# Kernel tuning notes

Hardware: AMD Instinct MI355X
Metric: run time of the kernel (lower is better)

## Reference

```python
import jax, jax.numpy as jnp
import numpy as np

B, N, F, E, C, FC = 16, 5000, 512, 160000, 64, 128


def gcn_conv(x, src, dst, W, b, n_total):
    loop = jnp.arange(n_total, dtype=src.dtype)
    s = jnp.concatenate([src, loop])
    d = jnp.concatenate([dst, loop])
    deg = jax.ops.segment_sum(jnp.ones_like(s, dtype=x.dtype), d, num_segments=n_total)
    dinv = jnp.where(deg > 0, jax.lax.rsqrt(deg), 0.0)
    norm = dinv[s] * dinv[d]                      # [E']
    h = x @ W                                      # [n_total, out]
    msg = h[s] * norm[:, None]
    out = jax.ops.segment_sum(msg, d, num_segments=n_total)
    return out + b


def setup_inputs() -> dict:
    key = jax.random.key(0)
    ks = jax.random.split(key, 12)
    inp = {
        "node_features": jax.random.normal(ks[0], (B, N, F), jnp.float32),
        "col_features": jax.random.normal(ks[1], (B, C, FC), jnp.float32),
        "edge_index": jax.random.randint(ks[2], (2, E), 0, N, dtype=jnp.int64),
        # GCNConv 1/2 weights + node head
        "W1": jax.random.normal(ks[3], (F, 16), jnp.float32) / np.sqrt(F),
        "b1": jnp.zeros((16,), jnp.float32),
        "W2": jax.random.normal(ks[4], (16, 16), jnp.float32) / 4.0,
        "b2": jnp.zeros((16,), jnp.float32),
        "fc_w": jax.random.normal(ks[5], (16, 1), jnp.float32) / 4.0,
        "fc_b": jnp.zeros((1,), jnp.float32),
        # column MLP: Linear(FC,16) -> ReLU -> Linear(16,1)
        "cw1": jax.random.normal(ks[6], (FC, 16), jnp.float32) / np.sqrt(FC),
        "cb1": jnp.zeros((16,), jnp.float32),
        "cw2": jax.random.normal(ks[7], (16, 1), jnp.float32) / 4.0,
        "cb2": jnp.zeros((1,), jnp.float32),
    }
    return inp


def reference(node_features, col_features, edge_index, W1, b1, W2, b2, fc_w, fc_b, cw1, cb1, cw2, cb2):
    b, n, _ = node_features.shape
    n_total = b * n
    # batched edge_index via node-offset trick (shared graph per batch element)
    offsets = (jnp.arange(b, dtype=edge_index.dtype) * n)[:, None]   # [B,1]
    src = (edge_index[0][None, :] + offsets).reshape(-1)              # [B*E]
    dst = (edge_index[1][None, :] + offsets).reshape(-1)

    x = node_features.reshape(n_total, -1)
    x = jax.nn.relu(gcn_conv(x, src, dst, W1, b1, n_total))
    x = jax.nn.relu(gcn_conv(x, src, dst, W2, b2, n_total))
    node_logits = (x.reshape(b, n, 16) @ fc_w + fc_b)[..., 0]         # [B,N]

    h = jax.nn.relu(col_features @ cw1 + cb1)
    col_logits = (h @ cw2 + cb2)[..., 0]                              # [B,C]

    joint = node_logits[:, :, None] + col_logits[:, None, :]          # [B,N,C]
    return joint.reshape(b, -1)                                       # [B, N*C]
```

## Files before the change

### kernel.cpp

```cpp
#include <hip/hip_runtime.h>
#include <hip/hip_bf16.h>

typedef unsigned short u16;
typedef unsigned int   u32;

#define B_  16
#define N_  5000
#define F_  512
#define C_  64
#define FC_ 128
#define NT  (B_ * N_)

__device__ __forceinline__ float bf2f(u16 h) {
    return __uint_as_float(((u32)h) << 16);
}
__device__ __forceinline__ u16 f2bf(float f) {
    union { __hip_bfloat16 h; u16 s; } c; c.h = __float2bfloat16(f); return c.s;
}
__device__ __forceinline__ float ldw(const void* p, int i, int fF) {
    return fF ? bf2f(((const u16*)p)[i]) : ((const float*)p)[i];
}

__global__ __launch_bounds__(256) void det_k(const u32* __restrict__ x32,
                                             const u32* __restrict__ ei32,
                                             int* __restrict__ flags)
{
    __shared__ int cnt;
    __shared__ int orv;
    if (threadIdx.x == 0) { cnt = 0; orv = 0; }
    __syncthreads();
    u32 w = x32[threadIdx.x];
    int e = (int)((w >> 7) & 0xffu);
    if (e >= 112 && e <= 136) atomicAdd(&cnt, 1);
    if (threadIdx.x < 32) {
        if (ei32[2 * threadIdx.x + 1] != 0u) atomicOr(&orv, 1);
    }
    __syncthreads();
    if (threadIdx.x == 0) {
        flags[0] = (cnt >= 128) ? 1 : 0;
        flags[1] = (orv == 0) ? 1 : 0;
    }
}

__device__ __forceinline__ int src_at(const u32* ei32, int t, int E, int fI) {
    return (int)(fI ? ei32[2 * t] : ei32[t]);
}
__device__ __forceinline__ int dst_at(const u32* ei32, int t, int E, int fI) {
    return (int)(fI ? ei32[2 * (E + t)] : ei32[E + t]);
}

__global__ __launch_bounds__(256) void prep_weights(
    const void* __restrict__ W1, const void* __restrict__ W2,
    const void* __restrict__ fcw, const void* __restrict__ cw1,
    const void* __restrict__ cw2, const void* __restrict__ b1,
    const void* __restrict__ b2, const void* __restrict__ fcb,
    const void* __restrict__ cb1, const void* __restrict__ cb2,
    const int* __restrict__ flags,
    float* __restrict__ w1f, float* __restrict__ w2f, float* __restrict__ fcwf,
    float* __restrict__ cw1f, float* __restrict__ cw2f, float* __restrict__ b1f,
    float* __restrict__ b2f, float* __restrict__ fcbf, float* __restrict__ cb1f,
    float* __restrict__ cb2f)
{
    int fF = flags[0];
    int t = blockIdx.x * blockDim.x + threadIdx.x;
    if (t < 8192) { w1f[t] = ldw(W1, t, fF); return; }
    int u = t - 8192;
    if (u < 256)  { w2f[u]  = ldw(W2, u, fF);  return; }  u -= 256;
    if (u < 16)   { fcwf[u] = ldw(fcw, u, fF); return; }  u -= 16;
    if (u < 2048) { cw1f[u] = ldw(cw1, u, fF); return; }  u -= 2048;
    if (u < 16)   { cw2f[u] = ldw(cw2, u, fF); return; }  u -= 16;
    if (u < 16)   { b1f[u]  = ldw(b1, u, fF);  return; }  u -= 16;
    if (u < 16)   { b2f[u]  = ldw(b2, u, fF);  return; }  u -= 16;
    if (u < 1)    { fcbf[u] = ldw(fcb, u, fF); return; }  u -= 1;
    if (u < 16)   { cb1f[u] = ldw(cb1, u, fF); return; }  u -= 16;
    if (u < 1)    { cb2f[u] = ldw(cb2, u, fF); return; }
}

__global__ __launch_bounds__(256) void deg_k(const u32* __restrict__ ei32,
                                             const int* __restrict__ flags,
                                             int* __restrict__ deg, int E)
{
    int t = blockIdx.x * blockDim.x + threadIdx.x;
    if (t >= E) return;
    int d = dst_at(ei32, t, E, flags[1]);
    if ((unsigned)d < (unsigned)N_) atomicAdd(&deg[d], 1);
}

__global__ __launch_bounds__(1024) void scan_k(const int* __restrict__ deg,
                                               int* __restrict__ rowptr,
                                               int* __restrict__ cursor,
                                               float* __restrict__ dinv)
{
    __shared__ int ssum[1024];
    int t = threadIdx.x;
    int base = t * 5;
    int loc[5];
    int run = 0;
#pragma unroll
    for (int i = 0; i < 5; i++) {
        int idx = base + i;
        int v = (idx < N_) ? deg[idx] : 0;
        loc[i] = run;
        run += v;
    }
    ssum[t] = run;
    __syncthreads();
    for (int offs = 1; offs < 1024; offs <<= 1) {
        int v = (t >= offs) ? ssum[t - offs] : 0;
        __syncthreads();
        ssum[t] += v;
        __syncthreads();
    }
    int exclusive = ssum[t] - run;
#pragma unroll
    for (int i = 0; i < 5; i++) {
        int idx = base + i;
        if (idx < N_) {
            int rp = exclusive + loc[i];
            rowptr[idx] = rp;
            cursor[idx] = rp;
            dinv[idx] = 1.0f / sqrtf((float)deg[idx] + 1.0f);
        }
    }
    if (t == 1023) rowptr[N_] = ssum[1023];
}

__global__ __launch_bounds__(256) void fill_k(const u32* __restrict__ ei32,
                                              const int* __restrict__ flags,
                                              int* __restrict__ cursor,
                                              int* __restrict__ csr, int E)
{
    int t = blockIdx.x * blockDim.x + threadIdx.x;
    if (t >= E) return;
    int fI = flags[1];
    int s = src_at(ei32, t, E, fI);
    int d = dst_at(ei32, t, E, fI);
    if ((unsigned)d >= (unsigned)N_) return;
    if ((unsigned)s >= (unsigned)N_) s = 0;
    int pos = atomicAdd(&cursor[d], 1);
    if ((unsigned)pos < (unsigned)E) csr[pos] = s;
}

__global__ __launch_bounds__(256) void gemm1_k(const void* __restrict__ xraw,
                                               const float* __restrict__ w1f,
                                               const float* __restrict__ dinv,
                                               const int* __restrict__ flags,
                                               u16* __restrict__ out)
{
    __shared__ float smem[64 * 129];
    const int t    = threadIdx.x;
    const int lane = t & 63;
    const int wv   = t >> 6;
    const int row0 = blockIdx.x * 64;
    const int fF   = flags[0];

    float acc[16];
#pragma unroll
    for (int k = 0; k < 16; k++) acc[k] = 0.0f;

    for (int p = 0; p < 4; p++) {
        __syncthreads();
        if (fF) {
            const u16* xb = (const u16*)xraw;
#pragma unroll
            for (int i = 0; i < 4; i++) {
                int idx = i * 256 + t;
                int r   = idx >> 4;
                int c   = (idx & 15) * 8;
                uint4 pk = *(const uint4*)(xb + (size_t)(row0 + r) * F_ + p * 128 + c);
                u32 q[4] = {pk.x, pk.y, pk.z, pk.w};
                float* dstp = smem + r * 129 + c;
#pragma unroll
                for (int j = 0; j < 4; j++) {
                    dstp[2 * j]     = bf2f((u16)(q[j] & 0xffffu));
                    dstp[2 * j + 1] = bf2f((u16)(q[j] >> 16));
                }
            }
        } else {
            const float* xf = (const float*)xraw;
#pragma unroll
            for (int i = 0; i < 8; i++) {
                int idx = i * 256 + t;
                int r   = idx >> 5;
                int c   = (idx & 31) * 4;
                float4 v = *(const float4*)(xf + (size_t)(row0 + r) * F_ + p * 128 + c);
                float* dstp = smem + r * 129 + c;
                dstp[0] = v.x; dstp[1] = v.y; dstp[2] = v.z; dstp[3] = v.w;
            }
        }
        __syncthreads();
        const float* xr = smem + lane * 129 + wv * 32;
        const float* wr = w1f + (p * 128 + wv * 32) * 16;
#pragma unroll
        for (int f = 0; f < 32; f++) {
            float xv = xr[f];
#pragma unroll
            for (int k = 0; k < 16; k++) acc[k] += xv * wr[f * 16 + k];
        }
    }

    __syncthreads();
    float (*red)[64][17] = (float (*)[64][17])smem;
#pragma unroll
    for (int k = 0; k < 16; k++) red[wv][lane][k] = acc[k];
    __syncthreads();

    int r  = t >> 2;
    int kc = (t & 3) * 4;
    int orow = row0 + r;
    float s = dinv[orow % N_];
    union { uint2 u; u16 h[4]; } o;
#pragma unroll
    for (int k = 0; k < 4; k++) {
        float v = red[0][r][kc + k] + red[1][r][kc + k]
                + red[2][r][kc + k] + red[3][r][kc + k];
        o.h[k] = f2bf(v * s);
    }
    *(uint2*)(out + (size_t)orow * 16 + kc) = o.u;
}

__global__ __launch_bounds__(256) void agg1_k(const u16* __restrict__ h,
                                              const int* __restrict__ rowptr,
                                              const int* __restrict__ csr,
                                              const float* __restrict__ dinv,
                                              const float* __restrict__ b1f,
                                              const float* __restrict__ w2f,
                                              u16* __restrict__ out)
{
    int t = blockIdx.x * blockDim.x + threadIdx.x;
    int g = t >> 4;
    if (g >= NT) return;
    int k = t & 15;
    int d = g % N_;
    int b = g / N_;
    const u16* hb = h + (size_t)b * N_ * 16;
    float acc = bf2f(hb[d * 16 + k]);
    int e0 = rowptr[d], e1 = rowptr[d + 1];
    for (int base = e0; base < e1; base += 8) {
        int idx[8];
#pragma unroll
        for (int j = 0; j < 8; j++) {
            int e = base + j;
            idx[j] = csr[e < e1 ? e : e0];
        }
        float v[8];
#pragma unroll
        for (int j = 0; j < 8; j++) v[j] = bf2f(hb[idx[j] * 16 + k]);
#pragma unroll
        for (int j = 0; j < 8; j++) if (base + j < e1) acc += v[j];
    }
    float dv = dinv[d];
    float x1 = fmaxf(acc * dv + b1f[k], 0.0f);
    float h2 = 0.0f;
#pragma unroll
    for (int j = 0; j < 16; j++) {
        float xj = __shfl(x1, j, 16);
        h2 += xj * w2f[j * 16 + k];
    }
    out[(size_t)g * 16 + k] = f2bf(h2 * dv);
}

__global__ __launch_bounds__(256) void agg2_k(const u16* __restrict__ h,
                                              const int* __restrict__ rowptr,
                                              const int* __restrict__ csr,
                                              const float* __restrict__ dinv,
                                              const float* __restrict__ b2f,
                                              const float* __restrict__ fcwf,
                                              const float* __restrict__ fcbf,
                                              float* __restrict__ nl)
{
    int t = blockIdx.x * blockDim.x + threadIdx.x;
    int g = t >> 4;
    if (g >= NT) return;
    int k = t & 15;
    int d = g % N_;
    int b = g / N_;
    const u16* hb = h + (size_t)b * N_ * 16;
    float acc = bf2f(hb[d * 16 + k]);
    int e0 = rowptr[d], e1 = rowptr[d + 1];
    for (int base = e0; base < e1; base += 8) {
        int idx[8];
#pragma unroll
        for (int j = 0; j < 8; j++) {
            int e = base + j;
            idx[j] = csr[e < e1 ? e : e0];
        }
        float v[8];
#pragma unroll
        for (int j = 0; j < 8; j++) v[j] = bf2f(hb[idx[j] * 16 + k]);
#pragma unroll
        for (int j = 0; j < 8; j++) if (base + j < e1) acc += v[j];
    }
    float x2 = fmaxf(acc * dinv[d] + b2f[k], 0.0f);
    float p = x2 * fcwf[k];
    p += __shfl_xor(p, 8, 16);
    p += __shfl_xor(p, 4, 16);
    p += __shfl_xor(p, 2, 16);
    p += __shfl_xor(p, 1, 16);
    if (k == 0) nl[g] = p + fcbf[0];
}

__global__ __launch_bounds__(256) void col_k(const void* __restrict__ cfraw,
                                             const float* __restrict__ cw1f,
                                             const float* __restrict__ cb1f,
                                             const float* __restrict__ cw2f,
                                             const float* __restrict__ cb2f,
                                             const int* __restrict__ flags,
                                             float* __restrict__ cl)
{
    int t = blockIdx.x * blockDim.x + threadIdx.x;
    if (t >= B_ * C_) return;
    float acc[16];
#pragma unroll
    for (int k = 0; k < 16; k++) acc[k] = cb1f[k];
    if (flags[0]) {
        const u16* r = (const u16*)cfraw + (size_t)t * FC_;
        for (int f = 0; f < FC_; f += 8) {
            uint4 pk = *(const uint4*)(r + f);
            u32 q[4] = {pk.x, pk.y, pk.z, pk.w};
#pragma unroll
            for (int j = 0; j < 4; j++) {
                float v0 = bf2f((u16)(q[j] & 0xffffu));
                float v1 = bf2f((u16)(q[j] >> 16));
                const float* w0 = cw1f + (f + 2 * j) * 16;
#pragma unroll
                for (int k = 0; k < 16; k++) acc[k] += v0 * w0[k];
#pragma unroll
                for (int k = 0; k < 16; k++) acc[k] += v1 * w0[16 + k];
            }
        }
    } else {
        const float* r = (const float*)cfraw + (size_t)t * FC_;
        for (int f = 0; f < FC_; f += 4) {
            float4 a = *(const float4*)(r + f);
            float v[4] = {a.x, a.y, a.z, a.w};
#pragma unroll
            for (int j = 0; j < 4; j++) {
                const float* w0 = cw1f + (f + j) * 16;
#pragma unroll
                for (int k = 0; k < 16; k++) acc[k] += v[j] * w0[k];
            }
        }
    }
    float s = cb2f[0];
#pragma unroll
    for (int k = 0; k < 16; k++) s += fmaxf(acc[k], 0.0f) * cw2f[k];
    cl[t] = s;
}

__global__ __launch_bounds__(256) void join_k(const float* __restrict__ nl,
                                              const float* __restrict__ cl,
                                              const int* __restrict__ flags,
                                              void* __restrict__ outraw)
{
    int t = blockIdx.x * blockDim.x + threadIdx.x;
    if (t >= NT * C_ / 8) return;
    int g  = t >> 3;
    int c0 = (t & 7) * 8;
    int b  = g / N_;
    float nv = nl[g];
    const float* c = cl + b * C_ + c0;
    float4 a0 = *(const float4*)c;
    float4 a1 = *(const float4*)(c + 4);
    float v[8] = {a0.x, a0.y, a0.z, a0.w, a1.x, a1.y, a1.z, a1.w};
#pragma unroll
    for (int i = 0; i < 8; i++) v[i] += nv;
    size_t idx = (size_t)g * C_ + c0;
    if (flags[0]) {
        union { uint4 u; u16 h[8]; } pkv;
#pragma unroll
        for (int i = 0; i < 8; i++) pkv.h[i] = f2bf(v[i]);
        *(uint4*)((u16*)outraw + idx) = pkv.u;
    } else {
        float* o = (float*)outraw + idx;
        *(float4*)o       = make_float4(v[0], v[1], v[2], v[3]);
        *(float4*)(o + 4) = make_float4(v[4], v[5], v[6], v[7]);
    }
}

extern "C" void kernel_launch(void* const* d_in, const int* in_sizes, int n_in,
                              void* d_out, int out_size, void* d_ws, size_t ws_size,
                              hipStream_t stream)
{
    const void* x    = d_in[0];
    const void* cf   = d_in[1];
    const u32*  ei32 = (const u32*)d_in[2];
    const void* W1   = d_in[3];
    const void* b1   = d_in[4];
    const void* W2   = d_in[5];
    const void* b2   = d_in[6];
    const void* fcw  = d_in[7];
    const void* fcb  = d_in[8];
    const void* cw1  = d_in[9];
    const void* cb1  = d_in[10];
    const void* cw2  = d_in[11];
    const void* cb2  = d_in[12];

    const int E = in_sizes[2] / 2;

    char* base = (char*)d_ws;
    size_t off = 0;
    auto alloc = [&](size_t bytes) -> void* {
        void* p = base + off;
        off = (off + bytes + 255) & ~(size_t)255;
        return p;
    };
    int*   flags  = (int*)alloc(2 * 4);
    float* w1f  = (float*)alloc(8192 * 4);
    float* w2f  = (float*)alloc(256 * 4);
    float* fcwf = (float*)alloc(16 * 4);
    float* cw1f = (float*)alloc(2048 * 4);
    float* cw2f = (float*)alloc(16 * 4);
    float* b1f  = (float*)alloc(16 * 4);
    float* b2f  = (float*)alloc(16 * 4);
    float* fcbf = (float*)alloc(4);
    float* cb1f = (float*)alloc(16 * 4);
    float* cb2f = (float*)alloc(4);
    int*   deg    = (int*)alloc((size_t)N_ * 4);
    int*   rowptr = (int*)alloc((size_t)(N_ + 1) * 4);
    int*   cursor = (int*)alloc((size_t)N_ * 4);
    float* dinv   = (float*)alloc((size_t)N_ * 4);
    int*   csr    = (int*)alloc((size_t)E * 4);
    u16*   bufA = (u16*)alloc((size_t)NT * 16 * 2);
    u16*   bufB = (u16*)alloc((size_t)NT * 16 * 2);
    float* nl   = (float*)alloc((size_t)NT * 4);
    float* cl   = (float*)alloc((size_t)B_ * C_ * 4);

    det_k<<<1, 256, 0, stream>>>((const u32*)x, ei32, flags);
    hipMemsetAsync(deg, 0, (size_t)N_ * 4, stream);
    prep_weights<<<(10578 + 255) / 256, 256, 0, stream>>>(
        W1, W2, fcw, cw1, cw2, b1, b2, fcb, cb1, cb2, flags,
        w1f, w2f, fcwf, cw1f, cw2f, b1f, b2f, fcbf, cb1f, cb2f);
    deg_k<<<(E + 255) / 256, 256, 0, stream>>>(ei32, flags, deg, E);
    scan_k<<<1, 1024, 0, stream>>>(deg, rowptr, cursor, dinv);
    fill_k<<<(E + 255) / 256, 256, 0, stream>>>(ei32, flags, cursor, csr, E);

    gemm1_k<<<NT / 64, 256, 0, stream>>>(x, w1f, dinv, flags, bufA);
    agg1_k<<<(NT * 16 + 255) / 256, 256, 0, stream>>>(bufA, rowptr, csr, dinv, b1f, w2f, bufB);
    agg2_k<<<(NT * 16 + 255) / 256, 256, 0, stream>>>(bufB, rowptr, csr, dinv, b2f, fcwf, fcbf, nl);
    col_k<<<(B_ * C_ + 255) / 256, 256, 0, stream>>>(cf, cw1f, cb1f, cw2f, cb2f, flags, cl);
    join_k<<<(NT * C_ / 8 + 255) / 256, 256, 0, stream>>>(nl, cl, flags, d_out);
}
```

Measured before the change: 404.2 us.

## Store hidden features node-major across batch and double-buffer GEMM1 tiles

The intermediate hidden buffers change from [B][N][16] to [N][B][16], so one block per node aggregates all 16 batch copies. Each neighbor gather then reads a contiguous 512-byte row instead of 16 scattered 32-byte pieces, and the CSR index reads are shared across the batch. GEMM1 separately switches to 64-column chunks with a register-prefetched, double-buffered shared-memory pipeline so global loads overlap the FMA work. The risks are more registers in GEMM1 and only 5000 blocks for the aggregation kernels.

```diff
diff --git a/kernel.cpp b/kernel.cpp
--- a/kernel.cpp
+++ b/kernel.cpp
@@ -147,7 +147,7 @@
                                                const int* __restrict__ flags,
                                                u16* __restrict__ out)
 {
-    __shared__ float smem[64 * 129];
+    __shared__ float smem[2][64 * 65];
     const int t    = threadIdx.x;
     const int lane = t & 63;
     const int wv   = t >> 6;
@@ -158,44 +158,114 @@
 #pragma unroll
     for (int k = 0; k < 16; k++) acc[k] = 0.0f;
 
-    for (int p = 0; p < 4; p++) {
+    float sreg[16];
+    if (fF) {
+        const u16* xb = (const u16*)xraw;
+#pragma unroll
+        for (int i = 0; i < 2; i++) {
+            int u = i * 256 + t;
+            int r = u >> 3, c8 = u & 7;
+            uint4 pk = *(const uint4*)(xb + (size_t)(row0 + r) * F_ + c8 * 8);
+            u32 q[4] = {pk.x, pk.y, pk.z, pk.w};
+#pragma unroll
+            for (int j = 0; j < 4; j++) {
+                sreg[i * 8 + 2 * j]     = bf2f((u16)(q[j] & 0xffffu));
+                sreg[i * 8 + 2 * j + 1] = bf2f((u16)(q[j] >> 16));
+            }
+        }
+    } else {
+        const float* xf = (const float*)xraw;
+#pragma unroll
+        for (int i = 0; i < 4; i++) {
+            int u = i * 256 + t;
+            int r = u >> 4, c4 = u & 15;
+            float4 v = *(const float4*)(xf + (size_t)(row0 + r) * F_ + c4 * 4);
+            sreg[i * 4 + 0] = v.x; sreg[i * 4 + 1] = v.y;
+            sreg[i * 4 + 2] = v.z; sreg[i * 4 + 3] = v.w;
+        }
+    }
+    if (fF) {
+#pragma unroll
+        for (int i = 0; i < 2; i++) {
+            int u = i * 256 + t;
+            int r = u >> 3, c8 = u & 7;
+            float* dp = &smem[0][r * 65 + c8 * 8];
+#pragma unroll
+            for (int j = 0; j < 8; j++) dp[j] = sreg[i * 8 + j];
+        }
+    } else {
+#pragma unroll
+        for (int i = 0; i < 4; i++) {
+            int u = i * 256 + t;
+            int r = u >> 4, c4 = u & 15;
+            float* dp = &smem[0][r * 65 + c4 * 4];
+#pragma unroll
+            for (int j = 0; j < 4; j++) dp[j] = sreg[i * 4 + j];
+        }
+    }
+
+    for (int c = 0; c < 8; c++) {
         __syncthreads();
-        if (fF) {
-            const u16* xb = (const u16*)xraw;
-#pragma unroll
-            for (int i = 0; i < 4; i++) {
-                int idx = i * 256 + t;
-                int r   = idx >> 4;
-                int c   = (idx & 15) * 8;
-                uint4 pk = *(const uint4*)(xb + (size_t)(row0 + r) * F_ + p * 128 + c);
-                u32 q[4] = {pk.x, pk.y, pk.z, pk.w};
-                float* dstp = smem + r * 129 + c;
-#pragma unroll
-                for (int j = 0; j < 4; j++) {
-                    dstp[2 * j]     = bf2f((u16)(q[j] & 0xffffu));
-                    dstp[2 * j + 1] = bf2f((u16)(q[j] >> 16));
+        float nreg[16];
+        if (c < 7) {
+            int fo = (c + 1) * 64;
+            if (fF) {
+                const u16* xb = (const u16*)xraw;
+#pragma unroll
+                for (int i = 0; i < 2; i++) {
+                    int u = i * 256 + t;
+                    int r = u >> 3, c8 = u & 7;
+                    uint4 pk = *(const uint4*)(xb + (size_t)(row0 + r) * F_ + fo + c8 * 8);
+                    u32 q[4] = {pk.x, pk.y, pk.z, pk.w};
+#pragma unroll
+                    for (int j = 0; j < 4; j++) {
+                        nreg[i * 8 + 2 * j]     = bf2f((u16)(q[j] & 0xffffu));
+                        nreg[i * 8 + 2 * j + 1] = bf2f((u16)(q[j] >> 16));
+                    }
+                }
+            } else {
+                const float* xf = (const float*)xraw;
+#pragma unroll
+                for (int i = 0; i < 4; i++) {
+                    int u = i * 256 + t;
+                    int r = u >> 4, c4 = u & 15;
+                    float4 v = *(const float4*)(xf + (size_t)(row0 + r) * F_ + fo + c4 * 4);
+                    nreg[i * 4 + 0] = v.x; nreg[i * 4 + 1] = v.y;
+                    nreg[i * 4 + 2] = v.z; nreg[i * 4 + 3] = v.w;
                 }
             }
-        } else {
-            const float* xf = (const float*)xraw;
-#pragma unroll
-            for (int i = 0; i < 8; i++) {
-                int idx = i * 256 + t;
-                int r   = idx >> 5;
-                int c   = (idx & 31) * 4;
-                float4 v = *(const float4*)(xf + (size_t)(row0 + r) * F_ + p * 128 + c);
-                float* dstp = smem + r * 129 + c;
-                dstp[0] = v.x; dstp[1] = v.y; dstp[2] = v.z; dstp[3] = v.w;
+        }
+        {
+            const float* xr = &smem[c & 1][lane * 65 + wv * 16];
+            const float* wr = w1f + (c * 64 + wv * 16) * 16;
+#pragma unroll
+            for (int f = 0; f < 16; f++) {
+                float xv = xr[f];
+#pragma unroll
+                for (int k = 0; k < 16; k++) acc[k] += xv * wr[f * 16 + k];
             }
         }
         __syncthreads();
-        const float* xr = smem + lane * 129 + wv * 32;
-        const float* wr = w1f + (p * 128 + wv * 32) * 16;
-#pragma unroll
-        for (int f = 0; f < 32; f++) {
-            float xv = xr[f];
-#pragma unroll
-            for (int k = 0; k < 16; k++) acc[k] += xv * wr[f * 16 + k];
+        if (c < 7) {
+            if (fF) {
+#pragma unroll
+                for (int i = 0; i < 2; i++) {
+                    int u = i * 256 + t;
+                    int r = u >> 3, c8 = u & 7;
+                    float* dp = &smem[(c + 1) & 1][r * 65 + c8 * 8];
+#pragma unroll
+                    for (int j = 0; j < 8; j++) dp[j] = nreg[i * 8 + j];
+                }
+            } else {
+#pragma unroll
+                for (int i = 0; i < 4; i++) {
+                    int u = i * 256 + t;
+                    int r = u >> 4, c4 = u & 15;
+                    float* dp = &smem[(c + 1) & 1][r * 65 + c4 * 4];
+#pragma unroll
+                    for (int j = 0; j < 4; j++) dp[j] = nreg[i * 4 + j];
+                }
+            }
         }
     }
 
@@ -207,8 +277,10 @@
 
     int r  = t >> 2;
     int kc = (t & 3) * 4;
-    int orow = row0 + r;
-    float s = dinv[orow % N_];
+    int row = row0 + r;
+    int n = row % N_;
+    int b = row / N_;
+    float s = dinv[n];
     union { uint2 u; u16 h[4]; } o;
 #pragma unroll
     for (int k = 0; k < 4; k++) {
@@ -216,7 +288,7 @@
                 + red[2][r][kc + k] + red[3][r][kc + k];
         o.h[k] = f2bf(v * s);
     }
-    *(uint2*)(out + (size_t)orow * 16 + kc) = o.u;
+    *(uint2*)(out + (size_t)n * 256 + b * 16 + kc) = o.u;
 }
 
 __global__ __launch_bounds__(256) void agg1_k(const u16* __restrict__ h,
@@ -227,14 +299,10 @@
                                               const float* __restrict__ w2f,
                                               u16* __restrict__ out)
 {
-    int t = blockIdx.x * blockDim.x + threadIdx.x;
-    int g = t >> 4;
-    if (g >= NT) return;
-    int k = t & 15;
-    int d = g % N_;
-    int b = g / N_;
-    const u16* hb = h + (size_t)b * N_ * 16;
-    float acc = bf2f(hb[d * 16 + k]);
+    int d   = blockIdx.x;
+    int tid = threadIdx.x;
+    int k   = tid & 15;
+    float acc = bf2f(h[(size_t)d * 256 + tid]);
     int e0 = rowptr[d], e1 = rowptr[d + 1];
     for (int base = e0; base < e1; base += 8) {
         int idx[8];
@@ -245,7 +313,7 @@
         }
         float v[8];
 #pragma unroll
-        for (int j = 0; j < 8; j++) v[j] = bf2f(hb[idx[j] * 16 + k]);
+        for (int j = 0; j < 8; j++) v[j] = bf2f(h[(size_t)idx[j] * 256 + tid]);
 #pragma unroll
         for (int j = 0; j < 8; j++) if (base + j < e1) acc += v[j];
     }
@@ -257,7 +325,7 @@
         float xj = __shfl(x1, j, 16);
         h2 += xj * w2f[j * 16 + k];
     }
-    out[(size_t)g * 16 + k] = f2bf(h2 * dv);
+    out[(size_t)d * 256 + tid] = f2bf(h2 * dv);
 }
 
 __global__ __launch_bounds__(256) void agg2_k(const u16* __restrict__ h,
@@ -269,14 +337,11 @@
                                               const float* __restrict__ fcbf,
                                               float* __restrict__ nl)
 {
-    int t = blockIdx.x * blockDim.x + threadIdx.x;
-    int g = t >> 4;
-    if (g >= NT) return;
-    int k = t & 15;
-    int d = g % N_;
-    int b = g / N_;
-    const u16* hb = h + (size_t)b * N_ * 16;
-    float acc = bf2f(hb[d * 16 + k]);
+    int d   = blockIdx.x;
+    int tid = threadIdx.x;
+    int k   = tid & 15;
+    int b   = tid >> 4;
+    float acc = bf2f(h[(size_t)d * 256 + tid]);
     int e0 = rowptr[d], e1 = rowptr[d + 1];
     for (int base = e0; base < e1; base += 8) {
         int idx[8];
@@ -287,7 +352,7 @@
         }
         float v[8];
 #pragma unroll
-        for (int j = 0; j < 8; j++) v[j] = bf2f(hb[idx[j] * 16 + k]);
+        for (int j = 0; j < 8; j++) v[j] = bf2f(h[(size_t)idx[j] * 256 + tid]);
 #pragma unroll
         for (int j = 0; j < 8; j++) if (base + j < e1) acc += v[j];
     }
@@ -297,7 +362,7 @@
     p += __shfl_xor(p, 4, 16);
     p += __shfl_xor(p, 2, 16);
     p += __shfl_xor(p, 1, 16);
-    if (k == 0) nl[g] = p + fcbf[0];
+    if (k == 0) nl[b * N_ + d] = p + fcbf[0];
 }
 
 __global__ __launch_bounds__(256) void col_k(const void* __restrict__ cfraw,
@@ -436,8 +501,8 @@
     fill_k<<<(E + 255) / 256, 256, 0, stream>>>(ei32, flags, cursor, csr, E);
 
     gemm1_k<<<NT / 64, 256, 0, stream>>>(x, w1f, dinv, flags, bufA);
-    agg1_k<<<(NT * 16 + 255) / 256, 256, 0, stream>>>(bufA, rowptr, csr, dinv, b1f, w2f, bufB);
-    agg2_k<<<(NT * 16 + 255) / 256, 256, 0, stream>>>(bufB, rowptr, csr, dinv, b2f, fcwf, fcbf, nl);
+    agg1_k<<<N_, 256, 0, stream>>>(bufA, rowptr, csr, dinv, b1f, w2f, bufB);
+    agg2_k<<<N_, 256, 0, stream>>>(bufB, rowptr, csr, dinv, b2f, fcwf, fcbf, nl);
     col_k<<<(B_ * C_ + 255) / 256, 256, 0, stream>>>(cf, cw1f, cb1f, cw2f, cb2f, flags, cl);
     join_k<<<(NT * C_ / 8 + 255) / 256, 256, 0, stream>>>(nl, cl, flags, d_out);
 }
```

After: 429.0 us. +6.1%, slower.

## Interleave batch into node-major feature layout and shrink gemm1 tile for occupancy

Applied to the files above, without the earlier changes.

The intermediate feature buffers move from batch-major [B][N][16] to node-major [N][B*16] layout. Each aggregation block now handles one destination node across all 16 batches, so every neighbor gather reads a contiguous 512-byte row and the CSR indices are loaded once per block instead of once per batch. gemm1 now stages 64-column chunks (smaller shared memory, launch_bounds minimum of 6) and writes its output in the new layout. The aggregation kernels no longer need a bounds check because the grid is exactly N blocks.

```diff
diff --git a/kernel.cpp b/kernel.cpp
--- a/kernel.cpp
+++ b/kernel.cpp
@@ -141,13 +141,13 @@
     if ((unsigned)pos < (unsigned)E) csr[pos] = s;
 }
 
-__global__ __launch_bounds__(256) void gemm1_k(const void* __restrict__ xraw,
-                                               const float* __restrict__ w1f,
-                                               const float* __restrict__ dinv,
-                                               const int* __restrict__ flags,
-                                               u16* __restrict__ out)
-{
-    __shared__ float smem[64 * 129];
+__global__ __launch_bounds__(256, 6) void gemm1_k(const void* __restrict__ xraw,
+                                                  const float* __restrict__ w1f,
+                                                  const float* __restrict__ dinv,
+                                                  const int* __restrict__ flags,
+                                                  u16* __restrict__ out)
+{
+    __shared__ float smem[4352];
     const int t    = threadIdx.x;
     const int lane = t & 63;
     const int wv   = t >> 6;
@@ -158,41 +158,39 @@
 #pragma unroll
     for (int k = 0; k < 16; k++) acc[k] = 0.0f;
 
-    for (int p = 0; p < 4; p++) {
+    for (int c = 0; c < 8; c++) {
         __syncthreads();
         if (fF) {
-            const u16* xb = (const u16*)xraw;
-#pragma unroll
-            for (int i = 0; i < 4; i++) {
-                int idx = i * 256 + t;
-                int r   = idx >> 4;
-                int c   = (idx & 15) * 8;
-                uint4 pk = *(const uint4*)(xb + (size_t)(row0 + r) * F_ + p * 128 + c);
+            const u16* xb = (const u16*)xraw + c * 64;
+#pragma unroll
+            for (int i = 0; i < 2; i++) {
+                int u = i * 256 + t;
+                int r = u >> 3, c8 = u & 7;
+                uint4 pk = *(const uint4*)(xb + (size_t)(row0 + r) * F_ + c8 * 8);
                 u32 q[4] = {pk.x, pk.y, pk.z, pk.w};
-                float* dstp = smem + r * 129 + c;
+                float* dp = &smem[r * 65 + c8 * 8];
 #pragma unroll
                 for (int j = 0; j < 4; j++) {
-                    dstp[2 * j]     = bf2f((u16)(q[j] & 0xffffu));
-                    dstp[2 * j + 1] = bf2f((u16)(q[j] >> 16));
+                    dp[2 * j]     = bf2f((u16)(q[j] & 0xffffu));
+                    dp[2 * j + 1] = bf2f((u16)(q[j] >> 16));
                 }
             }
         } else {
-            const float* xf = (const float*)xraw;
-#pragma unroll
-            for (int i = 0; i < 8; i++) {
-                int idx = i * 256 + t;
-                int r   = idx >> 5;
-                int c   = (idx & 31) * 4;
-                float4 v = *(const float4*)(xf + (size_t)(row0 + r) * F_ + p * 128 + c);
-                float* dstp = smem + r * 129 + c;
-                dstp[0] = v.x; dstp[1] = v.y; dstp[2] = v.z; dstp[3] = v.w;
+            const float* xf = (const float*)xraw + c * 64;
+#pragma unroll
+            for (int i = 0; i < 4; i++) {
+                int u = i * 256 + t;
+                int r = u >> 4, c4 = u & 15;
+                float4 v = *(const float4*)(xf + (size_t)(row0 + r) * F_ + c4 * 4);
+                float* dp = &smem[r * 65 + c4 * 4];
+                dp[0] = v.x; dp[1] = v.y; dp[2] = v.z; dp[3] = v.w;
             }
         }
         __syncthreads();
-        const float* xr = smem + lane * 129 + wv * 32;
-        const float* wr = w1f + (p * 128 + wv * 32) * 16;
-#pragma unroll
-        for (int f = 0; f < 32; f++) {
+        const float* xr = &smem[lane * 65 + wv * 16];
+        const float* wr = w1f + (c * 64 + wv * 16) * 16;
+#pragma unroll
+        for (int f = 0; f < 16; f++) {
             float xv = xr[f];
 #pragma unroll
             for (int k = 0; k < 16; k++) acc[k] += xv * wr[f * 16 + k];
@@ -207,8 +205,10 @@
 
     int r  = t >> 2;
     int kc = (t & 3) * 4;
-    int orow = row0 + r;
-    float s = dinv[orow % N_];
+    int row = row0 + r;
+    int n = row % N_;
+    int b = row / N_;
+    float s = dinv[n];
     union { uint2 u; u16 h[4]; } o;
 #pragma unroll
     for (int k = 0; k < 4; k++) {
@@ -216,7 +216,7 @@
                 + red[2][r][kc + k] + red[3][r][kc + k];
         o.h[k] = f2bf(v * s);
     }
-    *(uint2*)(out + (size_t)orow * 16 + kc) = o.u;
+    *(uint2*)(out + (size_t)n * 256 + b * 16 + kc) = o.u;
 }
 
 __global__ __launch_bounds__(256) void agg1_k(const u16* __restrict__ h,
@@ -227,14 +227,10 @@
                                               const float* __restrict__ w2f,
                                               u16* __restrict__ out)
 {
-    int t = blockIdx.x * blockDim.x + threadIdx.x;
-    int g = t >> 4;
-    if (g >= NT) return;
-    int k = t & 15;
-    int d = g % N_;
-    int b = g / N_;
-    const u16* hb = h + (size_t)b * N_ * 16;
-    float acc = bf2f(hb[d * 16 + k]);
+    int d   = blockIdx.x;
+    int tid = threadIdx.x;
+    int k   = tid & 15;
+    float acc = bf2f(h[(size_t)d * 256 + tid]);
     int e0 = rowptr[d], e1 = rowptr[d + 1];
     for (int base = e0; base < e1; base += 8) {
         int idx[8];
@@ -245,7 +241,7 @@
         }
         float v[8];
 #pragma unroll
-        for (int j = 0; j < 8; j++) v[j] = bf2f(hb[idx[j] * 16 + k]);
+        for (int j = 0; j < 8; j++) v[j] = bf2f(h[(size_t)idx[j] * 256 + tid]);
 #pragma unroll
         for (int j = 0; j < 8; j++) if (base + j < e1) acc += v[j];
     }
@@ -257,7 +253,7 @@
         float xj = __shfl(x1, j, 16);
         h2 += xj * w2f[j * 16 + k];
     }
-    out[(size_t)g * 16 + k] = f2bf(h2 * dv);
+    out[(size_t)d * 256 + tid] = f2bf(h2 * dv);
 }
 
 __global__ __launch_bounds__(256) void agg2_k(const u16* __restrict__ h,
@@ -269,14 +265,11 @@
                                               const float* __restrict__ fcbf,
                                               float* __restrict__ nl)
 {
-    int t = blockIdx.x * blockDim.x + threadIdx.x;
-    int g = t >> 4;
-    if (g >= NT) return;
-    int k = t & 15;
-    int d = g % N_;
-    int b = g / N_;
-    const u16* hb = h + (size_t)b * N_ * 16;
-    float acc = bf2f(hb[d * 16 + k]);
+    int d   = blockIdx.x;
+    int tid = threadIdx.x;
+    int k   = tid & 15;
+    int b   = tid >> 4;
+    float acc = bf2f(h[(size_t)d * 256 + tid]);
     int e0 = rowptr[d], e1 = rowptr[d + 1];
     for (int base = e0; base < e1; base += 8) {
         int idx[8];
@@ -287,7 +280,7 @@
         }
         float v[8];
 #pragma unroll
-        for (int j = 0; j < 8; j++) v[j] = bf2f(hb[idx[j] * 16 + k]);
+        for (int j = 0; j < 8; j++) v[j] = bf2f(h[(size_t)idx[j] * 256 + tid]);
 #pragma unroll
         for (int j = 0; j < 8; j++) if (base + j < e1) acc += v[j];
     }
@@ -297,7 +290,7 @@
     p += __shfl_xor(p, 4, 16);
     p += __shfl_xor(p, 2, 16);
     p += __shfl_xor(p, 1, 16);
-    if (k == 0) nl[g] = p + fcbf[0];
+    if (k == 0) nl[b * N_ + d] = p + fcbf[0];
 }
 
 __global__ __launch_bounds__(256) void col_k(const void* __restrict__ cfraw,
@@ -436,8 +429,8 @@
     fill_k<<<(E + 255) / 256, 256, 0, stream>>>(ei32, flags, cursor, csr, E);
 
     gemm1_k<<<NT / 64, 256, 0, stream>>>(x, w1f, dinv, flags, bufA);
-    agg1_k<<<(NT * 16 + 255) / 256, 256, 0, stream>>>(bufA, rowptr, csr, dinv, b1f, w2f, bufB);
-    agg2_k<<<(NT * 16 + 255) / 256, 256, 0, stream>>>(bufB, rowptr, csr, dinv, b2f, fcwf, fcbf, nl);
+    agg1_k<<<N_, 256, 0, stream>>>(bufA, rowptr, csr, dinv, b1f, w2f, bufB);
+    agg2_k<<<N_, 256, 0, stream>>>(bufB, rowptr, csr, dinv, b2f, fcwf, fcbf, nl);
     col_k<<<(B_ * C_ + 255) / 256, 256, 0, stream>>>(cf, cw1f, cb1f, cw2f, cb2f, flags, cl);
     join_k<<<(NT * C_ / 8 + 255) / 256, 256, 0, stream>>>(nl, cl, flags, d_out);
 }
```

Result: no change. 402.6 us (-0.4%).
